# Kernel tuning notes

Hardware: AMD Instinct MI355X
Metric: run time of the kernel (lower is better)

The kernel has to match this reference:

```python
import jax, jax.numpy as jnp
import numpy as np

N_NODES = 100000
N_EDGES = 3200000
D_IN = 256
D_OUT = 256


def setup_inputs() -> dict:
    key = jax.random.key(0)
    k1, k2, k3, k4, k5, k6 = jax.random.split(key, 6)
    bound = 1.0 / np.sqrt(D_OUT)
    x = jax.random.normal(k1, (N_NODES, D_IN), dtype=jnp.float32)
    weight = jax.random.uniform(k2, (D_IN, D_OUT), dtype=jnp.float32, minval=-bound, maxval=bound)
    bias = jax.random.uniform(k3, (D_OUT,), dtype=jnp.float32, minval=-bound, maxval=bound)
    edge_src = jax.random.randint(k4, (N_EDGES,), 0, N_NODES, dtype=jnp.int32)
    edge_dst = jax.random.randint(k5, (N_EDGES,), 0, N_NODES, dtype=jnp.int32)
    edge_weight = jax.random.uniform(k6, (N_EDGES,), dtype=jnp.float32)
    return {"x": x, "weight": weight, "bias": bias,
            "edge_src": edge_src, "edge_dst": edge_dst, "edge_weight": edge_weight}


def reference(x, weight, bias, edge_src, edge_dst, edge_weight):
    # XW = X @ W  -- dense GEMM, [N, D_out]
    xw = jnp.matmul(x, weight)
    # Z = A @ XW, A in COO: Z[dst] += w_e * XW[src]
    msgs = xw[edge_src] * edge_weight[:, None]          # [E, D_out] gather + scale
    z = jax.ops.segment_sum(msgs, edge_dst, num_segments=N_NODES)  # scatter-add
    return z + bias
```

## Files before the change

### kernel.cpp

```cpp
#include <hip/hip_runtime.h>
#include <hip/hip_bf16.h>
#include <stdint.h>

#define N_NODES 100000
#define N_EDGES 3200000
#define DDIM 256
#define NB 782
#define CAP 4800
#define BINBLK 4096
#define OCAP 65536

typedef __attribute__((ext_vector_type(8))) short short8v;
typedef __attribute__((ext_vector_type(4))) float f32x4;

static __device__ __forceinline__ unsigned short f32_to_bf16_rne(float f) {
  unsigned u = __float_as_uint(f);
  unsigned rounded = u + 0x7FFFu + ((u >> 16) & 1u);
  return (unsigned short)(rounded >> 16);
}

static __device__ __forceinline__ float bf16_to_f32(unsigned short h) {
  return __uint_as_float((unsigned)h << 16);
}

static __device__ __forceinline__ float bfLO(unsigned v) { return __uint_as_float(v << 16); }
static __device__ __forceinline__ float bfHI(unsigned v) { return __uint_as_float(v & 0xFFFF0000u); }


__global__ __launch_bounds__(256) void k_bin(const int* __restrict__ src,
                                             const int* __restrict__ dst,
                                             const float* __restrict__ w,
                                             int* __restrict__ bcur,
                                             uint2* __restrict__ bin,
                                             uint4* __restrict__ ofl,
                                             int* __restrict__ oflcnt) {
  __shared__ int hist[NB];
  const int t = threadIdx.x;
  const int e0 = blockIdx.x * BINBLK;
  int n = N_EDGES - e0;
  if (n > BINBLK) n = BINBLK;
  for (int i = t; i < NB; i += 256) hist[i] = 0;
  __syncthreads();
  int myd[16];
#pragma unroll
  for (int j = 0; j < 16; ++j) {
    int p = j * 256 + t;
    if (p < n) {
      myd[j] = dst[e0 + p];
      atomicAdd(&hist[myd[j] >> 7], 1);
    } else {
      myd[j] = -1;
    }
  }
  __syncthreads();
  for (int i = t; i < NB; i += 256) {
    int h = hist[i];
    hist[i] = h ? atomicAdd(&bcur[i * 16], h) : 0;
  }
  __syncthreads();
#pragma unroll
  for (int j = 0; j < 16; ++j) {
    int p = j * 256 + t;
    if (p < n) {
      int d = myd[j];
      int bkt = d >> 7;
      int q = atomicAdd(&hist[bkt], 1);
      if (q < CAP) {
        bin[(size_t)bkt * CAP + q] =
            make_uint2(((unsigned)(d & 127) << 17) | (unsigned)src[e0 + p],
                       __float_as_uint(w[e0 + p]));
      } else {
        int op = atomicAdd(oflcnt, 1);
        if (op < OCAP)
          ofl[op] = make_uint4((unsigned)d, (unsigned)src[e0 + p],
                               __float_as_uint(w[e0 + p]), 0u);
      }
    }
  }
}


__global__ __launch_bounds__(256) void k_cvtW(const float* __restrict__ w,
                                              unsigned short* __restrict__ wt) {
  int i = blockIdx.x * blockDim.x + threadIdx.x;
  int k = i >> 8;
  int n = i & 255;
  wt[(size_t)n * DDIM + k] = f32_to_bf16_rne(w[(size_t)k * DDIM + n]);
}


__global__ __launch_bounds__(512, 2) void k_gemm(const float* __restrict__ x,
                                                 const unsigned short* __restrict__ wt,
                                                 unsigned short* __restrict__ xw) {
  __shared__ unsigned short As[128 * 64];
  __shared__ unsigned short Bs[256 * 64];
  const int t = threadIdx.x;
  const int lane = t & 63;
  const int wid = t >> 6;
  const int wr = wid >> 1;
  const int wc = wid & 1;
  const int m0 = blockIdx.x * 128;

  f32x4 acc[2][8] = {};

  const int arow = t >> 2;
  const int akb = (t & 3) * 16;
  int am = m0 + arow;
  if (am > N_NODES - 1) am = N_NODES - 1;
  const int sr = t >> 3;
  const int sc = t & 7;

  const int kg = lane >> 4;
  const int rl = lane & 15;

  for (int kt = 0; kt < 4; ++kt) {
    const int k0 = kt * 64;
#pragma unroll
    for (int i = 0; i < 4; ++i) {
      int r = i * 64 + sr;
      int cc = sc ^ (r & 7);
      const unsigned short* srcp = wt + (size_t)r * DDIM + k0 + cc * 8;
      __builtin_amdgcn_global_load_lds(
          (const __attribute__((address_space(1))) void*)srcp,
          (__attribute__((address_space(3))) void*)((char*)Bs + i * 8192 + t * 16),
          16, 0, 0);
    }
    {
      const float* xp = x + (size_t)am * DDIM + k0 + akb;
      float4 f0 = *(const float4*)(xp + 0);
      float4 f1 = *(const float4*)(xp + 4);
      float4 f2 = *(const float4*)(xp + 8);
      float4 f3 = *(const float4*)(xp + 12);
      uint4 p0, p1;
      p0.x = (unsigned)f32_to_bf16_rne(f0.x) | ((unsigned)f32_to_bf16_rne(f0.y) << 16);
      p0.y = (unsigned)f32_to_bf16_rne(f0.z) | ((unsigned)f32_to_bf16_rne(f0.w) << 16);
      p0.z = (unsigned)f32_to_bf16_rne(f1.x) | ((unsigned)f32_to_bf16_rne(f1.y) << 16);
      p0.w = (unsigned)f32_to_bf16_rne(f1.z) | ((unsigned)f32_to_bf16_rne(f1.w) << 16);
      p1.x = (unsigned)f32_to_bf16_rne(f2.x) | ((unsigned)f32_to_bf16_rne(f2.y) << 16);
      p1.y = (unsigned)f32_to_bf16_rne(f2.z) | ((unsigned)f32_to_bf16_rne(f2.w) << 16);
      p1.z = (unsigned)f32_to_bf16_rne(f3.x) | ((unsigned)f32_to_bf16_rne(f3.y) << 16);
      p1.w = (unsigned)f32_to_bf16_rne(f3.z) | ((unsigned)f32_to_bf16_rne(f3.w) << 16);
      int b0 = arow * 128 + akb * 2;
      int swz = (arow & 7) << 4;
      *(uint4*)((char*)As + (b0 ^ swz)) = p0;
      *(uint4*)((char*)As + ((b0 + 16) ^ swz)) = p1;
    }
    __syncthreads();

#pragma unroll
    for (int ks = 0; ks < 2; ++ks) {
      const int colbyte = ks * 64 + kg * 16;
      short8v af[2];
#pragma unroll
      for (int mi = 0; mi < 2; ++mi) {
        int row = wr * 32 + mi * 16 + rl;
        int b = row * 128 + (colbyte ^ ((row & 7) << 4));
        af[mi] = *(const short8v*)((const char*)As + b);
      }
#pragma unroll
      for (int ni = 0; ni < 8; ++ni) {
        int row = wc * 128 + ni * 16 + rl;
        int b = row * 128 + (colbyte ^ ((row & 7) << 4));
        short8v bf = *(const short8v*)((const char*)Bs + b);
        acc[0][ni] = __builtin_amdgcn_mfma_f32_16x16x32_bf16(af[0], bf, acc[0][ni], 0, 0, 0);
        acc[1][ni] = __builtin_amdgcn_mfma_f32_16x16x32_bf16(af[1], bf, acc[1][ni], 0, 0, 0);
      }
    }
    __syncthreads();
  }

  const int rbase = (lane >> 4) * 4;
  const int ncol = lane & 15;
#pragma unroll
  for (int mi = 0; mi < 2; ++mi) {
#pragma unroll
    for (int ni = 0; ni < 8; ++ni) {
      int n = wc * 128 + ni * 16 + ncol;
#pragma unroll
      for (int r = 0; r < 4; ++r) {
        int m = m0 + wr * 32 + mi * 16 + rbase + r;
        if (m < N_NODES)
          xw[(size_t)m * DDIM + n] = f32_to_bf16_rne(acc[mi][ni][r]);
      }
    }
  }
}


__global__ __launch_bounds__(512, 8) void k_baggr(const uint2* __restrict__ bin,
                                                  const int* __restrict__ bcur,
                                                  const unsigned short* __restrict__ xw,
                                                  const float* __restrict__ bias,
                                                  float* __restrict__ z) {
  __shared__ uint2 srt[CAP];
  __shared__ int lh[129];
  __shared__ int lc[128];
  const int b = blockIdx.x;
  const int cb = blockIdx.y * 128;
  const int t = threadIdx.x;
  int cnt = bcur[b * 16];
  if (cnt > CAP) cnt = CAP;
  const int nbase = b << 7;
  int nmax = N_NODES - nbase;
  if (nmax > 128) nmax = 128;

  if (t < 129) lh[t] = 0;
  __syncthreads();

  const int wid = t >> 6;
  const int lane = t & 63;
  const int g = lane >> 4;
  const int l15 = lane & 15;
  const int gcol = cb + l15 * 8;
  const uint2* mybin = bin + (size_t)b * CAP;

  uint2 rec[10];
  int nrec = 0;
#pragma unroll
  for (int j = 0; j < 10; ++j) {
    int p = t + j * 512;
    if (p < cnt) {
      rec[j] = mybin[p];
      atomicAdd(&lh[(rec[j].x >> 17) + 1], 1);
      nrec = j + 1;
    }
  }
  __syncthreads();
  if (wid == 0) {
    int v0 = lh[lane + 1];
    int v1 = lh[lane + 65];
#pragma unroll
    for (int d = 1; d < 64; d <<= 1) {
      int u = __shfl_up(v0, d);
      if (lane >= d) v0 += u;
    }
    int tot0 = __shfl(v0, 63);
#pragma unroll
    for (int d = 1; d < 64; d <<= 1) {
      int u = __shfl_up(v1, d);
      if (lane >= d) v1 += u;
    }
    v1 += tot0;
    lh[lane + 1] = v0;
    lh[lane + 65] = v1;
  }
  __syncthreads();
  if (t < 128) lc[t] = lh[t];
  __syncthreads();
#pragma unroll
  for (int j = 0; j < 10; ++j) {
    if (j < nrec) {
      int q = atomicAdd(&lc[rec[j].x >> 17], 1);
      srt[q] = make_uint2(rec[j].x & 0x1FFFFu, rec[j].y);
    }
  }
  __syncthreads();

#pragma unroll 1
  for (int i = wid * 16; i < wid * 16 + 16; ++i) {
    if (i >= nmax) break;
    const int s = lh[i];
    const int e2 = lh[i + 1];
    float a0 = 0.f, a1 = 0.f, a2 = 0.f, a3 = 0.f;
    float a4 = 0.f, a5 = 0.f, a6 = 0.f, a7 = 0.f;
#pragma unroll 1
    for (int p = s; p < e2; p += 16) {
      unsigned sx0, sx1, sx2, sx3;
      float w0, w1, w2, w3;
      {
        int i0 = p + 0 * 4 + g; bool k0 = i0 < e2; uint2 r = srt[k0 ? i0 : s];
        sx0 = r.x; w0 = k0 ? __uint_as_float(r.y) : 0.f;
      }
      {
        int i1 = p + 1 * 4 + g; bool k1 = i1 < e2; uint2 r = srt[k1 ? i1 : s];
        sx1 = r.x; w1 = k1 ? __uint_as_float(r.y) : 0.f;
      }
      {
        int i2 = p + 2 * 4 + g; bool k2 = i2 < e2; uint2 r = srt[k2 ? i2 : s];
        sx2 = r.x; w2 = k2 ? __uint_as_float(r.y) : 0.f;
      }
      {
        int i3 = p + 3 * 4 + g; bool k3 = i3 < e2; uint2 r = srt[k3 ? i3 : s];
        sx3 = r.x; w3 = k3 ? __uint_as_float(r.y) : 0.f;
      }
      uint4 v0 = *(const uint4*)(xw + (size_t)sx0 * DDIM + gcol);
      uint4 v1 = *(const uint4*)(xw + (size_t)sx1 * DDIM + gcol);
      uint4 v2 = *(const uint4*)(xw + (size_t)sx2 * DDIM + gcol);
      uint4 v3 = *(const uint4*)(xw + (size_t)sx3 * DDIM + gcol);
      a0 += w0 * bfLO(v0.x); a1 += w0 * bfHI(v0.x);
      a2 += w0 * bfLO(v0.y); a3 += w0 * bfHI(v0.y);
      a4 += w0 * bfLO(v0.z); a5 += w0 * bfHI(v0.z);
      a6 += w0 * bfLO(v0.w); a7 += w0 * bfHI(v0.w);
      a0 += w1 * bfLO(v1.x); a1 += w1 * bfHI(v1.x);
      a2 += w1 * bfLO(v1.y); a3 += w1 * bfHI(v1.y);
      a4 += w1 * bfLO(v1.z); a5 += w1 * bfHI(v1.z);
      a6 += w1 * bfLO(v1.w); a7 += w1 * bfHI(v1.w);
      a0 += w2 * bfLO(v2.x); a1 += w2 * bfHI(v2.x);
      a2 += w2 * bfLO(v2.y); a3 += w2 * bfHI(v2.y);
      a4 += w2 * bfLO(v2.z); a5 += w2 * bfHI(v2.z);
      a6 += w2 * bfLO(v2.w); a7 += w2 * bfHI(v2.w);
      a0 += w3 * bfLO(v3.x); a1 += w3 * bfHI(v3.x);
      a2 += w3 * bfLO(v3.y); a3 += w3 * bfHI(v3.y);
      a4 += w3 * bfLO(v3.z); a5 += w3 * bfHI(v3.z);
      a6 += w3 * bfLO(v3.w); a7 += w3 * bfHI(v3.w);
    }
    a0 += __shfl_xor(a0, 16); a0 += __shfl_xor(a0, 32);
    a1 += __shfl_xor(a1, 16); a1 += __shfl_xor(a1, 32);
    a2 += __shfl_xor(a2, 16); a2 += __shfl_xor(a2, 32);
    a3 += __shfl_xor(a3, 16); a3 += __shfl_xor(a3, 32);
    a4 += __shfl_xor(a4, 16); a4 += __shfl_xor(a4, 32);
    a5 += __shfl_xor(a5, 16); a5 += __shfl_xor(a5, 32);
    a6 += __shfl_xor(a6, 16); a6 += __shfl_xor(a6, 32);
    a7 += __shfl_xor(a7, 16); a7 += __shfl_xor(a7, 32);
    if (g < 2) {
      const float4 bv = *(const float4*)(bias + gcol + (g ? 4 : 0));
      float4 o = g ? make_float4(a4 + bv.x, a5 + bv.y, a6 + bv.z, a7 + bv.w)
                   : make_float4(a0 + bv.x, a1 + bv.y, a2 + bv.z, a3 + bv.w);
      *(float4*)(z + (size_t)(nbase + i) * DDIM + gcol + (g ? 4 : 0)) = o;
    }
  }
}


__global__ __launch_bounds__(256) void k_ofl(const uint4* __restrict__ ofl,
                                             const int* __restrict__ oflcnt,
                                             const unsigned short* __restrict__ xw,
                                             float* __restrict__ z) {
  int n = oflcnt[0];
  if (n > OCAP) n = OCAP;
  for (int r = blockIdx.x; r < n; r += gridDim.x) {
    uint4 rec = ofl[r];
    float wgt = __uint_as_float(rec.z);
    int c = threadIdx.x;
    float v = bf16_to_f32(xw[(size_t)rec.y * DDIM + c]);
    atomicAdd(&z[(size_t)rec.x * DDIM + c], wgt * v);
  }
}

extern "C" void kernel_launch(void* const* d_in, const int* in_sizes, int n_in,
                              void* d_out, int out_size, void* d_ws, size_t ws_size,
                              hipStream_t stream) {
  const float* x = (const float*)d_in[0];
  const float* w = (const float*)d_in[1];
  const float* bias = (const float*)d_in[2];
  const int* esrc = (const int*)d_in[3];
  const int* edst = (const int*)d_in[4];
  const float* ew = (const float*)d_in[5];
  float* z = (float*)d_out;

  char* ws = (char*)d_ws;
  size_t off = 0;
  unsigned short* xw = (unsigned short*)(ws + off);
  off += (size_t)N_NODES * DDIM * 2;
  unsigned short* wt = (unsigned short*)(ws + off);
  off += (size_t)DDIM * DDIM * 2;
  int* bcur = (int*)(ws + off);
  off += (size_t)NB * 16 * 4;
  int* oflcnt = (int*)(ws + off);
  off += 256;
  uint4* ofl = (uint4*)(ws + off);
  off += (size_t)OCAP * 16;
  uint2* bin = (uint2*)(ws + off);
  off += (size_t)NB * CAP * 8;

  hipMemsetAsync(bcur, 0, (size_t)NB * 16 * 4 + 256, stream);
  k_bin<<<(N_EDGES + BINBLK - 1) / BINBLK, 256, 0, stream>>>(esrc, edst, ew, bcur, bin,
                                                             ofl, oflcnt);
  k_cvtW<<<(DDIM * DDIM + 255) / 256, 256, 0, stream>>>(w, wt);
  k_gemm<<<(N_NODES + 127) / 128, 512, 0, stream>>>(x, wt, xw);
  dim3 ag(NB, 2);
  k_baggr<<<ag, 512, 0, stream>>>(bin, bcur, xw, bias, z);
  k_ofl<<<64, 256, 0, stream>>>(ofl, oflcnt, xw, z);
}
```

Baseline: 407.0 us.

## Move per-bucket counting sort into separate kernel and split aggregation grid finer

The per-bucket counting sort by destination, previously redone inside each aggregation block (and duplicated across both column halves), now runs once in a new k_sort kernel. It writes sorted records and offsets to global memory. The aggregation kernel drops its large shared sort buffer and reads sorted edges straight from global memory. Its grid is split into 8 pieces per bucket (4 column quarters by 2 node halves, 256 threads), with 8 lanes per row and 8 edges in flight per step. This removes the redundant sort work and the shared memory that limited occupancy, at the cost of an extra kernel launch, an extra 25 MB binned-edge round trip, and more global reads of edge records per column slice.

```diff
diff --git a/kernel.cpp b/kernel.cpp
--- a/kernel.cpp
+++ b/kernel.cpp
@@ -9,6 +9,7 @@
 #define CAP 4800
 #define BINBLK 4096
 #define OCAP 65536
+#define NOFS 132
 
 typedef __attribute__((ext_vector_type(8))) short short8v;
 typedef __attribute__((ext_vector_type(4))) float f32x4;
@@ -77,6 +78,64 @@
       }
     }
   }
+}
+
+
+__global__ __launch_bounds__(512) void k_sort(const uint2* __restrict__ bin1,
+                                              const int* __restrict__ bcur,
+                                              uint2* __restrict__ bin2,
+                                              int* __restrict__ nof) {
+  __shared__ int lh[129];
+  __shared__ int lc[128];
+  const int b = blockIdx.x;
+  const int t = threadIdx.x;
+  int cnt = bcur[b * 16];
+  if (cnt > CAP) cnt = CAP;
+  if (t < 129) lh[t] = 0;
+  __syncthreads();
+  const int wid = t >> 6;
+  const int lane = t & 63;
+  uint2 rec[10];
+  int nrec = 0;
+#pragma unroll
+  for (int j = 0; j < 10; ++j) {
+    int p = t + j * 512;
+    if (p < cnt) {
+      rec[j] = bin1[(size_t)b * CAP + p];
+      atomicAdd(&lh[(rec[j].x >> 17) + 1], 1);
+      nrec = j + 1;
+    }
+  }
+  __syncthreads();
+  if (wid == 0) {
+    int v0 = lh[lane + 1];
+    int v1 = lh[lane + 65];
+#pragma unroll
+    for (int d = 1; d < 64; d <<= 1) {
+      int u = __shfl_up(v0, d);
+      if (lane >= d) v0 += u;
+    }
+    int tot0 = __shfl(v0, 63);
+#pragma unroll
+    for (int d = 1; d < 64; d <<= 1) {
+      int u = __shfl_up(v1, d);
+      if (lane >= d) v1 += u;
+    }
+    v1 += tot0;
+    lh[lane + 1] = v0;
+    lh[lane + 65] = v1;
+  }
+  __syncthreads();
+  if (t < 128) lc[t] = lh[t];
+  __syncthreads();
+#pragma unroll
+  for (int j = 0; j < 10; ++j) {
+    if (j < nrec) {
+      int q = atomicAdd(&lc[rec[j].x >> 17], 1);
+      bin2[(size_t)b * CAP + q] = rec[j];
+    }
+  }
+  if (t < 129) nof[b * NOFS + t] = lh[t];
 }
 
 
@@ -187,106 +246,59 @@
 }
 
 
-__global__ __launch_bounds__(512, 8) void k_baggr(const uint2* __restrict__ bin,
-                                                  const int* __restrict__ bcur,
+__global__ __launch_bounds__(256, 8) void k_baggr(const uint2* __restrict__ bin2,
+                                                  const int* __restrict__ nof,
                                                   const unsigned short* __restrict__ xw,
                                                   const float* __restrict__ bias,
                                                   float* __restrict__ z) {
-  __shared__ uint2 srt[CAP];
-  __shared__ int lh[129];
-  __shared__ int lc[128];
   const int b = blockIdx.x;
-  const int cb = blockIdx.y * 128;
+  const int q = blockIdx.y & 3;
+  const int h = blockIdx.y >> 2;
   const int t = threadIdx.x;
-  int cnt = bcur[b * 16];
-  if (cnt > CAP) cnt = CAP;
-  const int nbase = b << 7;
-  int nmax = N_NODES - nbase;
-  if (nmax > 128) nmax = 128;
-
-  if (t < 129) lh[t] = 0;
-  __syncthreads();
-
   const int wid = t >> 6;
   const int lane = t & 63;
-  const int g = lane >> 4;
-  const int l15 = lane & 15;
-  const int gcol = cb + l15 * 8;
-  const uint2* mybin = bin + (size_t)b * CAP;
-
-  uint2 rec[10];
-  int nrec = 0;
-#pragma unroll
-  for (int j = 0; j < 10; ++j) {
-    int p = t + j * 512;
-    if (p < cnt) {
-      rec[j] = mybin[p];
-      atomicAdd(&lh[(rec[j].x >> 17) + 1], 1);
-      nrec = j + 1;
-    }
-  }
-  __syncthreads();
-  if (wid == 0) {
-    int v0 = lh[lane + 1];
-    int v1 = lh[lane + 65];
-#pragma unroll
-    for (int d = 1; d < 64; d <<= 1) {
-      int u = __shfl_up(v0, d);
-      if (lane >= d) v0 += u;
-    }
-    int tot0 = __shfl(v0, 63);
-#pragma unroll
-    for (int d = 1; d < 64; d <<= 1) {
-      int u = __shfl_up(v1, d);
-      if (lane >= d) v1 += u;
-    }
-    v1 += tot0;
-    lh[lane + 1] = v0;
-    lh[lane + 65] = v1;
-  }
-  __syncthreads();
-  if (t < 128) lc[t] = lh[t];
-  __syncthreads();
-#pragma unroll
-  for (int j = 0; j < 10; ++j) {
-    if (j < nrec) {
-      int q = atomicAdd(&lc[rec[j].x >> 17], 1);
-      srt[q] = make_uint2(rec[j].x & 0x1FFFFu, rec[j].y);
-    }
-  }
-  __syncthreads();
+  const int g = lane >> 3;
+  const int l8 = lane & 7;
+  const int gofs = q * 64 + l8 * 8;
+  const uint2* mybin = bin2 + (size_t)b * CAP;
+  const int* myof = nof + b * NOFS + h * 64;
+
+  float4 bv = make_float4(0.f, 0.f, 0.f, 0.f);
+  if (g < 2) bv = *(const float4*)(bias + gofs + (g ? 4 : 0));
 
 #pragma unroll 1
-  for (int i = wid * 16; i < wid * 16 + 16; ++i) {
-    if (i >= nmax) break;
-    const int s = lh[i];
-    const int e2 = lh[i + 1];
+  for (int ii = 0; ii < 16; ++ii) {
+    const int i = wid * 16 + ii;
+    const int node = (b << 7) + h * 64 + i;
+    if (node >= N_NODES) break;
+    const int s = myof[i];
+    const int e2 = myof[i + 1];
     float a0 = 0.f, a1 = 0.f, a2 = 0.f, a3 = 0.f;
     float a4 = 0.f, a5 = 0.f, a6 = 0.f, a7 = 0.f;
 #pragma unroll 1
-    for (int p = s; p < e2; p += 16) {
+    for (int p = s; p < e2; p += 32) {
       unsigned sx0, sx1, sx2, sx3;
       float w0, w1, w2, w3;
       {
-        int i0 = p + 0 * 4 + g; bool k0 = i0 < e2; uint2 r = srt[k0 ? i0 : s];
-        sx0 = r.x; w0 = k0 ? __uint_as_float(r.y) : 0.f;
+        int i0 = p + 0 * 8 + g; bool k0 = i0 < e2; uint2 r = mybin[k0 ? i0 : s];
+        sx0 = r.x & 0x1FFFFu; w0 = k0 ? __uint_as_float(r.y) : 0.f;
       }
       {
-        int i1 = p + 1 * 4 + g; bool k1 = i1 < e2; uint2 r = srt[k1 ? i1 : s];
-        sx1 = r.x; w1 = k1 ? __uint_as_float(r.y) : 0.f;
+        int i1 = p + 1 * 8 + g; bool k1 = i1 < e2; uint2 r = mybin[k1 ? i1 : s];
+        sx1 = r.x & 0x1FFFFu; w1 = k1 ? __uint_as_float(r.y) : 0.f;
       }
       {
-        int i2 = p + 2 * 4 + g; bool k2 = i2 < e2; uint2 r = srt[k2 ? i2 : s];
-        sx2 = r.x; w2 = k2 ? __uint_as_float(r.y) : 0.f;
+        int i2 = p + 2 * 8 + g; bool k2 = i2 < e2; uint2 r = mybin[k2 ? i2 : s];
+        sx2 = r.x & 0x1FFFFu; w2 = k2 ? __uint_as_float(r.y) : 0.f;
       }
       {
-        int i3 = p + 3 * 4 + g; bool k3 = i3 < e2; uint2 r = srt[k3 ? i3 : s];
-        sx3 = r.x; w3 = k3 ? __uint_as_float(r.y) : 0.f;
-      }
-      uint4 v0 = *(const uint4*)(xw + (size_t)sx0 * DDIM + gcol);
-      uint4 v1 = *(const uint4*)(xw + (size_t)sx1 * DDIM + gcol);
-      uint4 v2 = *(const uint4*)(xw + (size_t)sx2 * DDIM + gcol);
-      uint4 v3 = *(const uint4*)(xw + (size_t)sx3 * DDIM + gcol);
+        int i3 = p + 3 * 8 + g; bool k3 = i3 < e2; uint2 r = mybin[k3 ? i3 : s];
+        sx3 = r.x & 0x1FFFFu; w3 = k3 ? __uint_as_float(r.y) : 0.f;
+      }
+      uint4 v0 = *(const uint4*)(xw + (size_t)sx0 * DDIM + gofs);
+      uint4 v1 = *(const uint4*)(xw + (size_t)sx1 * DDIM + gofs);
+      uint4 v2 = *(const uint4*)(xw + (size_t)sx2 * DDIM + gofs);
+      uint4 v3 = *(const uint4*)(xw + (size_t)sx3 * DDIM + gofs);
       a0 += w0 * bfLO(v0.x); a1 += w0 * bfHI(v0.x);
       a2 += w0 * bfLO(v0.y); a3 += w0 * bfHI(v0.y);
       a4 += w0 * bfLO(v0.z); a5 += w0 * bfHI(v0.z);
@@ -304,19 +316,18 @@
       a4 += w3 * bfLO(v3.z); a5 += w3 * bfHI(v3.z);
       a6 += w3 * bfLO(v3.w); a7 += w3 * bfHI(v3.w);
     }
-    a0 += __shfl_xor(a0, 16); a0 += __shfl_xor(a0, 32);
-    a1 += __shfl_xor(a1, 16); a1 += __shfl_xor(a1, 32);
-    a2 += __shfl_xor(a2, 16); a2 += __shfl_xor(a2, 32);
-    a3 += __shfl_xor(a3, 16); a3 += __shfl_xor(a3, 32);
-    a4 += __shfl_xor(a4, 16); a4 += __shfl_xor(a4, 32);
-    a5 += __shfl_xor(a5, 16); a5 += __shfl_xor(a5, 32);
-    a6 += __shfl_xor(a6, 16); a6 += __shfl_xor(a6, 32);
-    a7 += __shfl_xor(a7, 16); a7 += __shfl_xor(a7, 32);
+    a0 += __shfl_xor(a0, 8); a0 += __shfl_xor(a0, 16); a0 += __shfl_xor(a0, 32);
+    a1 += __shfl_xor(a1, 8); a1 += __shfl_xor(a1, 16); a1 += __shfl_xor(a1, 32);
+    a2 += __shfl_xor(a2, 8); a2 += __shfl_xor(a2, 16); a2 += __shfl_xor(a2, 32);
+    a3 += __shfl_xor(a3, 8); a3 += __shfl_xor(a3, 16); a3 += __shfl_xor(a3, 32);
+    a4 += __shfl_xor(a4, 8); a4 += __shfl_xor(a4, 16); a4 += __shfl_xor(a4, 32);
+    a5 += __shfl_xor(a5, 8); a5 += __shfl_xor(a5, 16); a5 += __shfl_xor(a5, 32);
+    a6 += __shfl_xor(a6, 8); a6 += __shfl_xor(a6, 16); a6 += __shfl_xor(a6, 32);
+    a7 += __shfl_xor(a7, 8); a7 += __shfl_xor(a7, 16); a7 += __shfl_xor(a7, 32);
     if (g < 2) {
-      const float4 bv = *(const float4*)(bias + gcol + (g ? 4 : 0));
       float4 o = g ? make_float4(a4 + bv.x, a5 + bv.y, a6 + bv.z, a7 + bv.w)
                    : make_float4(a0 + bv.x, a1 + bv.y, a2 + bv.z, a3 + bv.w);
-      *(float4*)(z + (size_t)(nbase + i) * DDIM + gcol + (g ? 4 : 0)) = o;
+      *(float4*)(z + (size_t)node * DDIM + gofs + (g ? 4 : 0)) = o;
     }
   }
 }
@@ -358,17 +369,22 @@
   off += (size_t)NB * 16 * 4;
   int* oflcnt = (int*)(ws + off);
   off += 256;
+  int* nof = (int*)(ws + off);
+  off += (size_t)NB * NOFS * 4;
   uint4* ofl = (uint4*)(ws + off);
   off += (size_t)OCAP * 16;
-  uint2* bin = (uint2*)(ws + off);
+  uint2* bin1 = (uint2*)(ws + off);
   off += (size_t)NB * CAP * 8;
+  uint2* bin2 = (uint2*)(ws + off);
+  off += (size_t)NB * CAP * 8;
 
   hipMemsetAsync(bcur, 0, (size_t)NB * 16 * 4 + 256, stream);
-  k_bin<<<(N_EDGES + BINBLK - 1) / BINBLK, 256, 0, stream>>>(esrc, edst, ew, bcur, bin,
+  k_bin<<<(N_EDGES + BINBLK - 1) / BINBLK, 256, 0, stream>>>(esrc, edst, ew, bcur, bin1,
                                                              ofl, oflcnt);
+  k_sort<<<NB, 512, 0, stream>>>(bin1, bcur, bin2, nof);
   k_cvtW<<<(DDIM * DDIM + 255) / 256, 256, 0, stream>>>(w, wt);
   k_gemm<<<(N_NODES + 127) / 128, 512, 0, stream>>>(x, wt, xw);
-  dim3 ag(NB, 2);
-  k_baggr<<<ag, 512, 0, stream>>>(bin, bcur, xw, bias, z);
+  dim3 ag(NB, 8);
+  k_baggr<<<ag, 256, 0, stream>>>(bin2, nof, xw, bias, z);
   k_ofl<<<64, 256, 0, stream>>>(ofl, oflcnt, xw, z);
 }
```

Result: slower. 451.9 us (+11.0%).
